# Optimization experiments

Measured on AMD Instinct MI355X. Metric: run time of the kernel, lower is better.

Reference implementation:

```python
import jax, jax.numpy as jnp
import numpy as np

N_TASK = 50000
N_EDGE = 50000
E = 500000
F_TASK = 64
F_EDGE = 64
H = 256
OUT = 256


def _lin(key, fan_in, fan_out):
    kw, kb = jax.random.split(key)
    lim = 1.0 / np.sqrt(fan_in)
    W = jax.random.uniform(kw, (fan_in, fan_out), minval=-lim, maxval=lim, dtype=jnp.float32)
    b = jax.random.uniform(kb, (fan_out,), minval=-lim, maxval=lim, dtype=jnp.float32)
    return W, b


def setup_inputs() -> dict:
    key = jax.random.key(0)
    ks = jax.random.split(key, 20)
    inp = {}
    inp['task_features'] = jax.random.normal(ks[0], (N_TASK, F_TASK), dtype=jnp.float32)
    inp['edge_features'] = jax.random.normal(ks[1], (N_EDGE, F_EDGE), dtype=jnp.float32)
    inp['queue_edges'] = jax.random.randint(ks[2], (2, E), 0, N_TASK)
    inp['type_edges'] = jax.random.randint(ks[3], (2, E), 0, N_TASK)
    inp['affinity_edges'] = jax.random.randint(ks[4], (2, E), 0, N_TASK)  # src<num_tasks, tgt<num_edges
    inp['topology_edges'] = jax.random.randint(ks[5], (2, E), 0, N_EDGE)
    inp['te_w1'], inp['te_b1'] = _lin(ks[6], F_TASK, H)
    inp['te_w2'], inp['te_b2'] = _lin(ks[7], H, H)
    inp['ee_w1'], inp['ee_b1'] = _lin(ks[8], F_EDGE, H)
    inp['ee_w2'], inp['ee_b2'] = _lin(ks[9], H, H)
    inp['gnn_w0'], inp['gnn_b0'] = _lin(ks[10], H, H)
    inp['gnn_w1'], inp['gnn_b1'] = _lin(ks[11], H, H)
    inp['ta_w'], inp['ta_b'] = _lin(ks[12], H, H)
    inp['ea_w'], inp['ea_b'] = _lin(ks[13], H, H)
    inp['out_w1'], inp['out_b1'] = _lin(ks[14], 2 * H, H)
    inp['out_w2'], inp['out_b2'] = _lin(ks[15], H, OUT)
    return inp


def _mean_msg(src_emb, src, tgt, num_segments):
    # scatter-add messages from src nodes into tgt slots, divide by in-degree (clamped >=1)
    msgs = jax.ops.segment_sum(src_emb[src], tgt, num_segments=num_segments)
    cnt = jax.ops.segment_sum(jnp.ones_like(src, dtype=src_emb.dtype), tgt, num_segments=num_segments)
    return msgs / jnp.maximum(cnt, 1.0)[:, None]


def _forward(task_features, edge_features, queue_edges, type_edges, affinity_edges, topology_edges,
             te_w1, te_b1, te_w2, te_b2, ee_w1, ee_b1, ee_w2, ee_b2,
             gnn_w0, gnn_b0, gnn_w1, gnn_b1, ta_w, ta_b, ea_w, ea_b,
             out_w1, out_b1, out_w2, out_b2):
    relu = jax.nn.relu
    # node encoders (Linear-ReLU-Linear-ReLU)
    t = relu(relu(task_features @ te_w1 + te_b1) @ te_w2 + te_b2)   # [N_task, H]
    e = relu(relu(edge_features @ ee_w1 + ee_b1) @ ee_w2 + ee_b2)   # [N_edge, H]

    # queue convolution: messages computed ONCE from original t (torch code never updates task_embeddings in loop)
    qs, qt = queue_edges[0], queue_edges[1]
    q_msgs = jax.ops.segment_sum(t[qs], qt, num_segments=t.shape[0])
    h = t
    for W, b in ((gnn_w0, gnn_b0), (gnn_w1, gnn_b1)):
        h = relu((h + 0.5 * q_msgs) @ W + b)
    t = h

    # type convolution: mean-aggregated same-type messages
    t = t + 0.3 * _mean_msg(t, type_edges[0], type_edges[1], t.shape[0])

    # affinity convolution: bipartite task<->edge exchange (simultaneous update)
    asrc, atgt = affinity_edges[0], affinity_edges[1]
    t_msgs = jax.ops.segment_sum(e[atgt], asrc, num_segments=t.shape[0])
    t_cnt = jax.ops.segment_sum(jnp.ones((asrc.shape[0],), t.dtype), asrc, num_segments=t.shape[0])
    e_msgs = jax.ops.segment_sum(t[asrc], atgt, num_segments=e.shape[0])
    e_cnt = jax.ops.segment_sum(jnp.ones((atgt.shape[0],), e.dtype), atgt, num_segments=e.shape[0])
    t_new = t + 0.3 * t_msgs / jnp.maximum(t_cnt, 1.0)[:, None]
    e_new = e + 0.3 * e_msgs / jnp.maximum(e_cnt, 1.0)[:, None]
    t, e = t_new, e_new

    # topology convolution: edge-edge mean aggregation
    e = e + 0.3 * _mean_msg(e, topology_edges[0], topology_edges[1], e.shape[0])

    # graph-level aggregation
    t_agg = relu(jnp.mean(t, axis=0) @ ta_w + ta_b)  # [H]
    e_agg = relu(jnp.mean(e, axis=0) @ ea_w + ea_b)  # [H]
    combined = jnp.concatenate([t_agg, e_agg], axis=0)  # [2H]
    out = relu(combined @ out_w1 + out_b1) @ out_w2 + out_b2  # [OUT]
    return out


def reference(task_features, edge_features, queue_edges, type_edges, affinity_edges, topology_edges,
              te_w1, te_b1, te_w2, te_b2, ee_w1, ee_b1, ee_w2, ee_b2,
              gnn_w0, gnn_b0, gnn_w1, gnn_b1, ta_w, ta_b, ea_w, ea_b,
              out_w1, out_b1, out_w2, out_b2):
    return _forward(task_features, edge_features, queue_edges, type_edges, affinity_edges, topology_edges,
                    te_w1, te_b1, te_w2, te_b2, ee_w1, ee_b1, ee_w2, ee_b2,
                    gnn_w0, gnn_b0, gnn_w1, gnn_b1, ta_w, ta_b, ea_w, ea_b,
                    out_w1, out_b1, out_w2, out_b2)
```

## Files before the change

### kernel.cpp

```cpp
#include <hip/hip_runtime.h>

#define H 256
#define NT 50000
#define NEDGE 50000
#define NE 500000

#define NBKT 391
#define NBLK 123
#define CHUNK 4096
#define CAP 2816

typedef __attribute__((ext_vector_type(8))) short short8_t;
typedef __attribute__((ext_vector_type(4))) float f32x4;
typedef unsigned short u16;
typedef unsigned int u32;

__device__ __forceinline__ float b2f(u16 v) { return __uint_as_float((u32)v << 16); }
__device__ __forceinline__ u16 f2b(float f) {
    u32 u = __float_as_uint(f);
    u += 0x7FFFu + ((u >> 16) & 1u);
    return (u16)(u >> 16);
}

__device__ __forceinline__ u32 f2fp8_1(float f) {
    u32 u = __float_as_uint(f);
    u32 s = (u >> 24) & 0x80u;
    float af = fabsf(f);
    if (af >= 448.f) return s | 0x7Eu;
    if (af < 0.015625f) {
        int m = (int)rintf(af * 512.0f);
        return s | (u32)m;
    }
    u32 au = __float_as_uint(af);
    u32 r = au + 0x7FFFFu + ((au >> 20) & 1u);
    int e = (int)(r >> 23) - 127;
    return s | (u32)(((e + 7) << 3) | ((r >> 20) & 7u));
}
__device__ __forceinline__ float fp82f_1(u32 b) {
    u32 s = (b & 0x80u) << 24;
    u32 em = b & 0x7Fu;
    float v;
    if (em >= 8) v = __uint_as_float((((em >> 3) + 120u) << 23) | ((em & 7u) << 20));
    else v = (float)em * 0.001953125f;
    return __uint_as_float(__float_as_uint(v) | s);
}
__device__ __forceinline__ u32 pk4_fp8(float a, float b, float c, float d) {
#if __has_builtin(__builtin_amdgcn_cvt_pk_fp8_f32)
    u32 r = 0;
    r = (u32)__builtin_amdgcn_cvt_pk_fp8_f32(a, b, (int)r, false);
    r = (u32)__builtin_amdgcn_cvt_pk_fp8_f32(c, d, (int)r, true);
    return r;
#else
    return f2fp8_1(a) | (f2fp8_1(b) << 8) | (f2fp8_1(c) << 16) | (f2fp8_1(d) << 24);
#endif
}
__device__ __forceinline__ float4 unpk4_fp8(u32 v) {
#if __has_builtin(__builtin_amdgcn_cvt_pk_f32_fp8)
    auto lo = __builtin_amdgcn_cvt_pk_f32_fp8(v, false);
    auto hi = __builtin_amdgcn_cvt_pk_f32_fp8(v, true);
    return make_float4(lo[0], lo[1], hi[0], hi[1]);
#else
    return make_float4(fp82f_1(v & 255u), fp82f_1((v >> 8) & 255u),
                       fp82f_1((v >> 16) & 255u), fp82f_1(v >> 24));
#endif
}

__device__ __forceinline__ const int* pick_list(
    int l, const int* a, const int* b, const int* c, const int* d, const int* e)
{ return (l == 0) ? a : (l == 1) ? b : (l == 2) ? c : (l == 3) ? d : e; }

__device__ __forceinline__ void enc_body(
    char* arena, int bid, const float* __restrict__ X,
    const u16* __restrict__ W1h, const u16* __restrict__ W1l, const float* __restrict__ b1,
    const u16* __restrict__ W2h, const u16* __restrict__ W2l, const float* __restrict__ b2,
    u16* __restrict__ out, u32* __restrict__ f8, int N)
{
    const int m0 = bid * 64;

    for (int i = threadIdx.x; i < 64 * 8; i += 256) {
        int r = i >> 3, c8 = i & 7;
        int gr = m0 + r; if (gr >= N) gr = N - 1;
        const float* xf = X + (size_t)gr * 64 + c8 * 8;
        float4 a = *(const float4*)xf;
        float4 b = *(const float4*)(xf + 4);
        uint4 v;
        v.x = (u32)f2b(a.x) | ((u32)f2b(a.y) << 16);
        v.y = (u32)f2b(a.z) | ((u32)f2b(a.w) << 16);
        v.z = (u32)f2b(b.x) | ((u32)f2b(b.y) << 16);
        v.w = (u32)f2b(b.z) | ((u32)f2b(b.w) << 16);
        u32 byte = (u32)(r * 128 + c8 * 16) ^ (u32)((r & 7) << 4);
        *(uint4*)(arena + byte) = v;
    }
    __syncthreads();

    const int wv = threadIdx.x >> 6, l = threadIdx.x & 63;
    const int li = l & 15, lk = l >> 4;

    f32x4 acc[4][4];
    #pragma unroll
    for (int i = 0; i < 4; i++)
        #pragma unroll
        for (int j = 0; j < 4; j++)
            acc[i][j] = (f32x4){0.f, 0.f, 0.f, 0.f};

    {
        short8_t whc[4], wlc[4];
        #pragma unroll
        for (int ni = 0; ni < 4; ni++) {
            const size_t wi = (size_t)((wv * 4 + ni) * 2) * 64 + l;
            whc[ni] = ((const short8_t*)W1h)[wi];
            wlc[ni] = ((const short8_t*)W1l)[wi];
        }
        #pragma unroll
        for (int ks = 0; ks < 2; ks++) {
            short8_t whn[4], wln[4];
            if (ks + 1 < 2) {
                #pragma unroll
                for (int ni = 0; ni < 4; ni++) {
                    const size_t wi = (size_t)((wv * 4 + ni) * 2 + ks + 1) * 64 + l;
                    whn[ni] = ((const short8_t*)W1h)[wi];
                    wln[ni] = ((const short8_t*)W1l)[wi];
                }
            }
            short8_t xb[4];
            #pragma unroll
            for (int mi = 0; mi < 4; mi++) {
                int m = mi * 16 + li;
                u32 byte = (u32)(m * 128 + (ks * 32 + lk * 8) * 2) ^ (u32)((m & 7) << 4);
                xb[mi] = *(const short8_t*)(arena + byte);
            }
            __builtin_amdgcn_s_setprio(1);
            #pragma unroll
            for (int ni = 0; ni < 4; ni++)
                #pragma unroll
                for (int mi = 0; mi < 4; mi++) {
                    acc[mi][ni] = __builtin_amdgcn_mfma_f32_16x16x32_bf16(wlc[ni], xb[mi], acc[mi][ni], 0, 0, 0);
                    acc[mi][ni] = __builtin_amdgcn_mfma_f32_16x16x32_bf16(whc[ni], xb[mi], acc[mi][ni], 0, 0, 0);
                }
            __builtin_amdgcn_s_setprio(0);
            if (ks + 1 < 2) {
                #pragma unroll
                for (int ni = 0; ni < 4; ni++) { whc[ni] = whn[ni]; wlc[ni] = wln[ni]; }
            }
        }
    }

    __syncthreads();

    #pragma unroll
    for (int ni = 0; ni < 4; ni++) {
        int c = wv * 64 + ni * 16 + lk * 4;
        float4 b4 = *(const float4*)(b1 + c);
        #pragma unroll
        for (int mi = 0; mi < 4; mi++) {
            int m = mi * 16 + li;
            float o0 = fmaxf(acc[mi][ni][0] + b4.x, 0.f);
            float o1 = fmaxf(acc[mi][ni][1] + b4.y, 0.f);
            float o2 = fmaxf(acc[mi][ni][2] + b4.z, 0.f);
            float o3 = fmaxf(acc[mi][ni][3] + b4.w, 0.f);
            u32 w0 = (u32)f2b(o0) | ((u32)f2b(o1) << 16);
            u32 w1 = (u32)f2b(o2) | ((u32)f2b(o3) << 16);
            u32 byte = (u32)(m * 512 + c * 2) ^ (u32)((m & 7) << 4);
            *(uint2*)(arena + byte) = make_uint2(w0, w1);
        }
    }
    __syncthreads();

    #pragma unroll
    for (int i = 0; i < 4; i++)
        #pragma unroll
        for (int j = 0; j < 4; j++)
            acc[i][j] = (f32x4){0.f, 0.f, 0.f, 0.f};

    {
        short8_t whc[4], wlc[4];
        #pragma unroll
        for (int ni = 0; ni < 4; ni++) {
            const size_t wi = (size_t)((wv * 4 + ni) * 8) * 64 + l;
            whc[ni] = ((const short8_t*)W2h)[wi];
            wlc[ni] = ((const short8_t*)W2l)[wi];
        }
        #pragma unroll
        for (int ks = 0; ks < 8; ks++) {
            short8_t whn[4], wln[4];
            if (ks + 1 < 8) {
                #pragma unroll
                for (int ni = 0; ni < 4; ni++) {
                    const size_t wi = (size_t)((wv * 4 + ni) * 8 + ks + 1) * 64 + l;
                    whn[ni] = ((const short8_t*)W2h)[wi];
                    wln[ni] = ((const short8_t*)W2l)[wi];
                }
            }
            short8_t xb[4];
            #pragma unroll
            for (int mi = 0; mi < 4; mi++) {
                int m = mi * 16 + li;
                u32 byte = (u32)(m * 512 + (ks * 32 + lk * 8) * 2) ^ (u32)((m & 7) << 4);
                xb[mi] = *(const short8_t*)(arena + byte);
            }
            __builtin_amdgcn_s_setprio(1);
            #pragma unroll
            for (int ni = 0; ni < 4; ni++)
                #pragma unroll
                for (int mi = 0; mi < 4; mi++) {
                    acc[mi][ni] = __builtin_amdgcn_mfma_f32_16x16x32_bf16(wlc[ni], xb[mi], acc[mi][ni], 0, 0, 0);
                    acc[mi][ni] = __builtin_amdgcn_mfma_f32_16x16x32_bf16(whc[ni], xb[mi], acc[mi][ni], 0, 0, 0);
                }
            __builtin_amdgcn_s_setprio(0);
            if (ks + 1 < 8) {
                #pragma unroll
                for (int ni = 0; ni < 4; ni++) { whc[ni] = whn[ni]; wlc[ni] = wln[ni]; }
            }
        }
    }

    __syncthreads();
    #pragma unroll
    for (int ni = 0; ni < 4; ni++) {
        int c = wv * 64 + ni * 16 + lk * 4;
        float4 b4 = *(const float4*)(b2 + c);
        #pragma unroll
        for (int mi = 0; mi < 4; mi++) {
            int m = mi * 16 + li;
            float o0 = fmaxf(acc[mi][ni][0] + b4.x, 0.f);
            float o1 = fmaxf(acc[mi][ni][1] + b4.y, 0.f);
            float o2 = fmaxf(acc[mi][ni][2] + b4.z, 0.f);
            float o3 = fmaxf(acc[mi][ni][3] + b4.w, 0.f);
            u32 w0 = (u32)f2b(o0) | ((u32)f2b(o1) << 16);
            u32 w1 = (u32)f2b(o2) | ((u32)f2b(o3) << 16);
            u32 byte = (u32)(m * 512 + c * 2) ^ (u32)((m & 7) << 4);
            *(uint2*)(arena + byte) = make_uint2(w0, w1);
        }
    }
    __syncthreads();
    for (int i = threadIdx.x; i < 64 * 32; i += 256) {
        int r = i >> 5, c8 = i & 31;
        int m = m0 + r;
        if (m < N) {
            u32 byte = (u32)(r * 512 + c8 * 16) ^ (u32)((r & 7) << 4);
            uint4 v = *(const uint4*)(arena + byte);
            *(uint4*)(out + (size_t)m * H + c8 * 8) = v;
            u32 p0 = pk4_fp8(b2f((u16)(v.x & 0xFFFF)), b2f((u16)(v.x >> 16)),
                             b2f((u16)(v.y & 0xFFFF)), b2f((u16)(v.y >> 16)));
            u32 p1 = pk4_fp8(b2f((u16)(v.z & 0xFFFF)), b2f((u16)(v.z >> 16)),
                             b2f((u16)(v.w & 0xFFFF)), b2f((u16)(v.w >> 16)));
            *(uint2*)(f8 + (size_t)m * 64 + c8 * 2) = make_uint2(p0, p1);
        }
    }
}

__global__ __launch_bounds__(256) void part_enc(
    const int* __restrict__ k0, const int* __restrict__ k1, const int* __restrict__ k2,
    const int* __restrict__ k3, const int* __restrict__ k4,
    const int* __restrict__ v0, const int* __restrict__ v1, const int* __restrict__ v2,
    const int* __restrict__ v3, const int* __restrict__ v4,
    const int* __restrict__ starts, int* __restrict__ csr,
    const float* __restrict__ X,
    const u16* __restrict__ W1h, const u16* __restrict__ W1l, const float* __restrict__ b1,
    const u16* __restrict__ W2h, const u16* __restrict__ W2l, const float* __restrict__ b2,
    u16* __restrict__ out, u32* __restrict__ f8, int N, int nCSR)
{
    __shared__ char arena[32768];
    if ((int)blockIdx.x >= nCSR) {
        enc_body(arena, blockIdx.x - nCSR, X, W1h, W1l, b1, W2h, W2l, b2, out, f8, N);
        return;
    }
    u32* ent = (u32*)arena;
    u16* ebk = (u16*)(arena + 16384);
    int* cnt  = (int*)(arena + 24576);
    int* loff = cnt + NBKT;
    int* cur  = loff + NBKT;
    int* gst  = cur + NBKT;
    int* buf  = (int*)(arena + 24576 + 4 * 4 * NBKT);
    int p = blockIdx.x;
    int l = p / NBLK, blk = p % NBLK;
    int t = threadIdx.x;
    const int* k = pick_list(l, k0, k1, k2, k3, k4);
    const int* v = pick_list(l, v0, v1, v2, v3, v4);
    const int* st = starts + ((size_t)l * NBLK + blk) * NBKT;
    for (int i = t; i < NBKT; i += 256) { cnt[i] = 0; gst[i] = st[i]; }
    __syncthreads();
    int e0 = blk * CHUNK;
    u32 ep[16]; int eb[16];
    #pragma unroll
    for (int j = 0; j < 16; j++) {
        int e = e0 + j * 256 + t;
        if (e < NE) {
            int key = k[e];
            eb[j] = key >> 7;
            ep[j] = ((u32)(key & 127) << 16) | (u32)v[e];
            atomicAdd(&cnt[eb[j]], 1);
        } else eb[j] = -1;
    }
    __syncthreads();
    int b0 = t * 2;
    int c0 = (b0 < NBKT) ? cnt[b0] : 0;
    int c1 = (b0 + 1 < NBKT) ? cnt[b0 + 1] : 0;
    int s = c0 + c1;
    buf[t] = s; __syncthreads();
    for (int stp = 1; stp < 256; stp <<= 1) {
        int x = (t >= stp) ? buf[t - stp] : 0; __syncthreads();
        buf[t] += x; __syncthreads();
    }
    int run = buf[t] - s;
    if (b0 < NBKT)     { loff[b0] = run;          cur[b0] = run; }
    if (b0 + 1 < NBKT) { loff[b0 + 1] = run + c0; cur[b0 + 1] = run + c0; }
    __syncthreads();
    #pragma unroll
    for (int j = 0; j < 16; j++) {
        if (eb[j] >= 0) {
            int q = atomicAdd(&cur[eb[j]], 1);
            ent[q] = ep[j]; ebk[q] = (u16)eb[j];
        }
    }
    __syncthreads();
    int nv = min(CHUNK, NE - e0);
    int* c = csr + (size_t)l * NE;
    for (int i = t; i < nv; i += 256) {
        int b = ebk[i];
        c[gst[b] + (i - loff[b])] = (int)ent[i];
    }
}

__global__ __launch_bounds__(256) void buck_enc(
    const int* __restrict__ bases, int* __restrict__ csr, int* __restrict__ off,
    const float* __restrict__ X,
    const u16* __restrict__ W1h, const u16* __restrict__ W1l, const float* __restrict__ b1,
    const u16* __restrict__ W2h, const u16* __restrict__ W2l, const float* __restrict__ b2,
    u16* __restrict__ out, u32* __restrict__ f8, int N, int nCSR)
{
    __shared__ char arena[32768];
    if ((int)blockIdx.x >= nCSR) {
        enc_body(arena, blockIdx.x - nCSR, X, W1h, W1l, b1, W2h, W2l, b2, out, f8, N);
        return;
    }
    int* seg  = (int*)arena;
    int* hist = (int*)(arena + 11264);
    int* scn  = hist + 128;
    int p = blockIdx.x;
    int l = p / NBKT, b = p % NBKT;
    int t = threadIdx.x;
    int base = bases[l * (NBKT + 1) + b];
    int end  = bases[l * (NBKT + 1) + b + 1];
    int sz = end - base; if (sz > CAP) sz = CAP;
    int* c = csr + (size_t)l * NE;
    for (int i = t; i < sz; i += 256) seg[i] = c[base + i];
    if (t < 128) hist[t] = 0;
    __syncthreads();
    for (int i = t; i < sz; i += 256) atomicAdd(&hist[seg[i] >> 16], 1);
    __syncthreads();
    if (t < 128) scn[t] = hist[t];
    __syncthreads();
    for (int st = 1; st < 128; st <<= 1) {
        int v = 0;
        if (t < 128 && t >= st) v = scn[t - st];
        __syncthreads();
        if (t < 128) scn[t] += v;
        __syncthreads();
    }
    if (t < 128) {
        int key = b * 128 + t;
        int excl = scn[t] - hist[t];
        if (key < NT) off[l * (NT + 1) + key] = base + excl;
        hist[t] = excl;
    }
    if (b == 0 && t == 128) off[l * (NT + 1) + NT] = NE;
    __syncthreads();
    for (int i = t; i < sz; i += 256) {
        int u = seg[i];
        int q = atomicAdd(&hist[u >> 16], 1);
        c[base + q] = u & 0xFFFF;
    }
}

template<int K1>
__global__ __launch_bounds__(256) void fused_mlp(
    const u16* __restrict__ X, const u16* __restrict__ Q,
    const u16* __restrict__ W1h, const u16* __restrict__ W1l, const float* __restrict__ b1,
    const u16* __restrict__ W2h, const u16* __restrict__ W2l, const float* __restrict__ b2,
    u16* __restrict__ out, u32* __restrict__ f8,
    int N, float s2)
{
    __shared__ u16 lds[64 * 256];
    const int m0 = blockIdx.x * 64;

    constexpr int RCH = K1 / 8;
    for (int i = threadIdx.x; i < 64 * RCH; i += 256) {
        int r = i / RCH, c8 = i % RCH;
        int gr = m0 + r; if (gr >= N) gr = N - 1;
        uint4 v = *(const uint4*)(X + (size_t)gr * K1 + c8 * 8);
        u32 byte = (u32)(r * (K1 * 2) + c8 * 16) ^ (u32)((r & 7) << 4);
        *(uint4*)((char*)lds + byte) = v;
    }
    __syncthreads();

    const int wv = threadIdx.x >> 6, l = threadIdx.x & 63;
    const int li = l & 15, lk = l >> 4;

    f32x4 acc[4][4];
    #pragma unroll
    for (int i = 0; i < 4; i++)
        #pragma unroll
        for (int j = 0; j < 4; j++)
            acc[i][j] = (f32x4){0.f, 0.f, 0.f, 0.f};

    {
        constexpr int KS = K1 / 32;
        short8_t whc[4], wlc[4];
        #pragma unroll
        for (int ni = 0; ni < 4; ni++) {
            const size_t wi = (size_t)((wv * 4 + ni) * KS) * 64 + l;
            whc[ni] = ((const short8_t*)W1h)[wi];
            wlc[ni] = ((const short8_t*)W1l)[wi];
        }
        #pragma unroll
        for (int ks = 0; ks < KS; ks++) {
            short8_t whn[4], wln[4];
            if (ks + 1 < KS) {
                #pragma unroll
                for (int ni = 0; ni < 4; ni++) {
                    const size_t wi = (size_t)((wv * 4 + ni) * KS + ks + 1) * 64 + l;
                    whn[ni] = ((const short8_t*)W1h)[wi];
                    wln[ni] = ((const short8_t*)W1l)[wi];
                }
            }
            short8_t xb[4];
            #pragma unroll
            for (int mi = 0; mi < 4; mi++) {
                int m = mi * 16 + li;
                u32 byte = (u32)(m * (K1 * 2) + (ks * 32 + lk * 8) * 2) ^ (u32)((m & 7) << 4);
                xb[mi] = *(const short8_t*)((const char*)lds + byte);
            }
            __builtin_amdgcn_s_setprio(1);
            #pragma unroll
            for (int ni = 0; ni < 4; ni++)
                #pragma unroll
                for (int mi = 0; mi < 4; mi++) {
                    acc[mi][ni] = __builtin_amdgcn_mfma_f32_16x16x32_bf16(wlc[ni], xb[mi], acc[mi][ni], 0, 0, 0);
                    acc[mi][ni] = __builtin_amdgcn_mfma_f32_16x16x32_bf16(whc[ni], xb[mi], acc[mi][ni], 0, 0, 0);
                }
            __builtin_amdgcn_s_setprio(0);
            if (ks + 1 < KS) {
                #pragma unroll
                for (int ni = 0; ni < 4; ni++) { whc[ni] = whn[ni]; wlc[ni] = wln[ni]; }
            }
        }
    }

    __syncthreads();

    #pragma unroll
    for (int ni = 0; ni < 4; ni++) {
        int c = wv * 64 + ni * 16 + lk * 4;
        float4 b4 = *(const float4*)(b1 + c);
        #pragma unroll
        for (int mi = 0; mi < 4; mi++) {
            int m = mi * 16 + li;
            float o0 = fmaxf(acc[mi][ni][0] + b4.x, 0.f);
            float o1 = fmaxf(acc[mi][ni][1] + b4.y, 0.f);
            float o2 = fmaxf(acc[mi][ni][2] + b4.z, 0.f);
            float o3 = fmaxf(acc[mi][ni][3] + b4.w, 0.f);
            int gm = m0 + m; if (gm >= N) gm = N - 1;
            uint2 qv = *(const uint2*)(Q + (size_t)gm * 256 + c);
            o0 = fmaf(s2, b2f((u16)(qv.x & 0xFFFF)), o0);
            o1 = fmaf(s2, b2f((u16)(qv.x >> 16)), o1);
            o2 = fmaf(s2, b2f((u16)(qv.y & 0xFFFF)), o2);
            o3 = fmaf(s2, b2f((u16)(qv.y >> 16)), o3);
            u32 w0 = (u32)f2b(o0) | ((u32)f2b(o1) << 16);
            u32 w1 = (u32)f2b(o2) | ((u32)f2b(o3) << 16);
            u32 byte = (u32)(m * 512 + c * 2) ^ (u32)((m & 7) << 4);
            *(uint2*)((char*)lds + byte) = make_uint2(w0, w1);
        }
    }
    __syncthreads();

    #pragma unroll
    for (int i = 0; i < 4; i++)
        #pragma unroll
        for (int j = 0; j < 4; j++)
            acc[i][j] = (f32x4){0.f, 0.f, 0.f, 0.f};

    {
        short8_t whc[4], wlc[4];
        #pragma unroll
        for (int ni = 0; ni < 4; ni++) {
            const size_t wi = (size_t)((wv * 4 + ni) * 8) * 64 + l;
            whc[ni] = ((const short8_t*)W2h)[wi];
            wlc[ni] = ((const short8_t*)W2l)[wi];
        }
        #pragma unroll
        for (int ks = 0; ks < 8; ks++) {
            short8_t whn[4], wln[4];
            if (ks + 1 < 8) {
                #pragma unroll
                for (int ni = 0; ni < 4; ni++) {
                    const size_t wi = (size_t)((wv * 4 + ni) * 8 + ks + 1) * 64 + l;
                    whn[ni] = ((const short8_t*)W2h)[wi];
                    wln[ni] = ((const short8_t*)W2l)[wi];
                }
            }
            short8_t xb[4];
            #pragma unroll
            for (int mi = 0; mi < 4; mi++) {
                int m = mi * 16 + li;
                u32 byte = (u32)(m * 512 + (ks * 32 + lk * 8) * 2) ^ (u32)((m & 7) << 4);
                xb[mi] = *(const short8_t*)((const char*)lds + byte);
            }
            __builtin_amdgcn_s_setprio(1);
            #pragma unroll
            for (int ni = 0; ni < 4; ni++)
                #pragma unroll
                for (int mi = 0; mi < 4; mi++) {
                    acc[mi][ni] = __builtin_amdgcn_mfma_f32_16x16x32_bf16(wlc[ni], xb[mi], acc[mi][ni], 0, 0, 0);
                    acc[mi][ni] = __builtin_amdgcn_mfma_f32_16x16x32_bf16(whc[ni], xb[mi], acc[mi][ni], 0, 0, 0);
                }
            __builtin_amdgcn_s_setprio(0);
            if (ks + 1 < 8) {
                #pragma unroll
                for (int ni = 0; ni < 4; ni++) { whc[ni] = whn[ni]; wlc[ni] = wln[ni]; }
            }
        }
    }

    __syncthreads();
    #pragma unroll
    for (int ni = 0; ni < 4; ni++) {
        int c = wv * 64 + ni * 16 + lk * 4;
        float4 b4 = *(const float4*)(b2 + c);
        #pragma unroll
        for (int mi = 0; mi < 4; mi++) {
            int m = mi * 16 + li;
            float o0 = fmaxf(acc[mi][ni][0] + b4.x, 0.f);
            float o1 = fmaxf(acc[mi][ni][1] + b4.y, 0.f);
            float o2 = fmaxf(acc[mi][ni][2] + b4.z, 0.f);
            float o3 = fmaxf(acc[mi][ni][3] + b4.w, 0.f);
            u32 w0 = (u32)f2b(o0) | ((u32)f2b(o1) << 16);
            u32 w1 = (u32)f2b(o2) | ((u32)f2b(o3) << 16);
            u32 byte = (u32)(m * 512 + c * 2) ^ (u32)((m & 7) << 4);
            *(uint2*)((char*)lds + byte) = make_uint2(w0, w1);
        }
    }
    __syncthreads();
    for (int i = threadIdx.x; i < 64 * 32; i += 256) {
        int r = i >> 5, c8 = i & 31;
        int m = m0 + r;
        if (m < N) {
            u32 byte = (u32)(r * 512 + c8 * 16) ^ (u32)((r & 7) << 4);
            uint4 v = *(const uint4*)((const char*)lds + byte);
            *(uint4*)(out + (size_t)m * H + c8 * 8) = v;
            u32 p0 = pk4_fp8(b2f((u16)(v.x & 0xFFFF)), b2f((u16)(v.x >> 16)),
                             b2f((u16)(v.y & 0xFFFF)), b2f((u16)(v.y >> 16)));
            u32 p1 = pk4_fp8(b2f((u16)(v.z & 0xFFFF)), b2f((u16)(v.z >> 16)),
                             b2f((u16)(v.w & 0xFFFF)), b2f((u16)(v.w >> 16)));
            *(uint2*)(f8 + (size_t)m * 64 + c8 * 2) = make_uint2(p0, p1);
        }
    }
}

__global__ __launch_bounds__(256) void wt_pack(
    const float* __restrict__ s0, const float* __restrict__ s1,
    const float* __restrict__ s2, const float* __restrict__ s3,
    const float* __restrict__ s4, const float* __restrict__ s5,
    u16* __restrict__ arena)
{
    const int li = blockIdx.y;
    const int K = (li == 0 || li == 4) ? 64 : 256;
    const int offs[6] = {0, 32768, 163840, 294912, 425984, 458752};
    int n = K * 256;
    int i = blockIdx.x * 256 + threadIdx.x;
    if (i >= n) return;
    const float* W = (li == 0) ? s0 : (li == 1) ? s1 : (li == 2) ? s2
                   : (li == 3) ? s3 : (li == 4) ? s4 : s5;
    u16* hi = arena + offs[li];
    u16* lo = hi + n;
    int k = i >> 8, c = i & 255;
    float u = W[i];
    u32 b = __float_as_uint(u);
    float r = u - __uint_as_float(b & 0xFFFF0000u);
    int lane = ((k >> 3) & 3) * 16 + (c & 15);
    size_t idx = ((size_t)((c >> 4) * (K >> 5) + (k >> 5)) * 64 + lane) * 8 + (k & 7);
    hi[idx] = (u16)(b >> 16);
    lo[idx] = f2b(r);
}

__global__ __launch_bounds__(256) void hist_kernel(
    const int* __restrict__ k0, const int* __restrict__ k1, const int* __restrict__ k2,
    const int* __restrict__ k3, const int* __restrict__ k4, int* __restrict__ counts)
{
    __shared__ int h[NBKT];
    int l = blockIdx.y;
    const int* k = pick_list(l, k0, k1, k2, k3, k4);
    for (int i = threadIdx.x; i < NBKT; i += 256) h[i] = 0;
    __syncthreads();
    int e0 = blockIdx.x * CHUNK;
    for (int i = threadIdx.x; i < CHUNK; i += 256) {
        int e = e0 + i;
        if (e < NE) atomicAdd(&h[k[e] >> 7], 1);
    }
    __syncthreads();
    int* out = counts + ((size_t)l * NBLK + blockIdx.x) * NBKT;
    for (int i = threadIdx.x; i < NBKT; i += 256) out[i] = h[i];
}

__global__ __launch_bounds__(256) void scan_buckets(
    const int* __restrict__ counts, int* __restrict__ starts, int* __restrict__ bases)
{
    __shared__ int buf[256];
    int l = blockIdx.x, t = threadIdx.x;
    const int* cl = counts + (size_t)l * NBLK * NBKT;
    int* sl = starts + (size_t)l * NBLK * NBKT;
    int b0 = t * 2;
    int totloc[2];
    int s = 0;
    #pragma unroll
    for (int j = 0; j < 2; j++) {
        int b = b0 + j, v = 0;
        if (b < NBKT) for (int k = 0; k < NBLK; k++) v += cl[k * NBKT + b];
        totloc[j] = v; s += v;
    }
    buf[t] = s; __syncthreads();
    for (int st = 1; st < 256; st <<= 1) {
        int v = (t >= st) ? buf[t - st] : 0; __syncthreads();
        buf[t] += v; __syncthreads();
    }
    int run = buf[t] - s;
    #pragma unroll
    for (int j = 0; j < 2; j++) {
        int b = b0 + j;
        if (b < NBKT) {
            bases[l * (NBKT + 1) + b] = run;
            int p = run;
            for (int k = 0; k < NBLK; k++) { sl[k * NBKT + b] = p; p += cl[k * NBKT + b]; }
            run += totloc[j];
        }
    }
    if (t == 255) bases[l * (NBKT + 1) + NBKT] = NE;
}

__global__ __launch_bounds__(256) void gather_q_f8(
    const u32* __restrict__ src, const int* __restrict__ csr,
    const int* __restrict__ off, const u16* __restrict__ baseT,
    u16* __restrict__ sumOut, u16* __restrict__ fuseOut, float s2, int N)
{
    int r = (blockIdx.x * 256 + threadIdx.x) >> 6;
    int lane = threadIdx.x & 63;
    if (r >= N) return;
    int o0 = off[r];
    int d  = off[r + 1] - o0;
    float4 acc = {0.f, 0.f, 0.f, 0.f};
    int j = 0;
    for (; j + 8 <= d; j += 8) {
        u32 w[8];
        #pragma unroll
        for (int q = 0; q < 8; q++)
            w[q] = src[(size_t)csr[o0 + j + q] * 64 + lane];
        #pragma unroll
        for (int q = 0; q < 8; q++) {
            float4 f = unpk4_fp8(w[q]);
            acc.x += f.x; acc.y += f.y; acc.z += f.z; acc.w += f.w;
        }
    }
    for (; j < d; j++) {
        float4 f = unpk4_fp8(src[(size_t)csr[o0 + j] * 64 + lane]);
        acc.x += f.x; acc.y += f.y; acc.z += f.z; acc.w += f.w;
    }
    ushort4 pk;
    pk.x = f2b(acc.x); pk.y = f2b(acc.y); pk.z = f2b(acc.z); pk.w = f2b(acc.w);
    ((ushort4*)(sumOut + (size_t)r * H))[lane] = pk;
    ushort4 b = ((const ushort4*)(baseT + (size_t)r * H))[lane];
    pk.x = f2b(fmaf(s2, acc.x, b2f(b.x)));
    pk.y = f2b(fmaf(s2, acc.y, b2f(b.y)));
    pk.z = f2b(fmaf(s2, acc.z, b2f(b.z)));
    pk.w = f2b(fmaf(s2, acc.w, b2f(b.w)));
    ((ushort4*)(fuseOut + (size_t)r * H))[lane] = pk;
}

__global__ __launch_bounds__(256) void gather_task2(
    const u32* __restrict__ M1s, const int* __restrict__ csr1, const int* __restrict__ off1,
    const u32* __restrict__ M2s, const int* __restrict__ csr2, const int* __restrict__ off2,
    const u16* __restrict__ T, u16* __restrict__ Sout, u32* __restrict__ M3out, int N)
{
    int r = (blockIdx.x * 256 + threadIdx.x) >> 6;
    int lane = threadIdx.x & 63;
    if (r >= N) return;

    float4 a1 = {0.f, 0.f, 0.f, 0.f};
    {
        int o0 = off1[r], d = off1[r + 1] - o0;
        int j = 0;
        for (; j + 8 <= d; j += 8) {
            u32 w[8];
            #pragma unroll
            for (int q = 0; q < 8; q++)
                w[q] = M1s[(size_t)csr1[o0 + j + q] * 64 + lane];
            #pragma unroll
            for (int q = 0; q < 8; q++) {
                float4 f = unpk4_fp8(w[q]);
                a1.x += f.x; a1.y += f.y; a1.z += f.z; a1.w += f.w;
            }
        }
        for (; j < d; j++) {
            float4 f = unpk4_fp8(M1s[(size_t)csr1[o0 + j] * 64 + lane]);
            a1.x += f.x; a1.y += f.y; a1.z += f.z; a1.w += f.w;
        }
        float s = 0.3f / (float)max(d, 1);
        a1.x *= s; a1.y *= s; a1.z *= s; a1.w *= s;
    }
    float4 a2 = {0.f, 0.f, 0.f, 0.f};
    {
        int o0 = off2[r], d = off2[r + 1] - o0;
        int j = 0;
        for (; j + 8 <= d; j += 8) {
            u32 w[8];
            #pragma unroll
            for (int q = 0; q < 8; q++)
                w[q] = M2s[(size_t)csr2[o0 + j + q] * 64 + lane];
            #pragma unroll
            for (int q = 0; q < 8; q++) {
                float4 f = unpk4_fp8(w[q]);
                a2.x += f.x; a2.y += f.y; a2.z += f.z; a2.w += f.w;
            }
        }
        for (; j < d; j++) {
            float4 f = unpk4_fp8(M2s[(size_t)csr2[o0 + j] * 64 + lane]);
            a2.x += f.x; a2.y += f.y; a2.z += f.z; a2.w += f.w;
        }
        float s = 0.3f / (float)max(d, 1);
        a2.x *= s; a2.y *= s; a2.z *= s; a2.w *= s;
    }
    ushort4 b = ((const ushort4*)(T + (size_t)r * H))[lane];
    float f0 = b2f(b.x) + a1.x, f1 = b2f(b.y) + a1.y;
    float f2 = b2f(b.z) + a1.z, f3 = b2f(b.w) + a1.w;
    M3out[(size_t)r * 64 + lane] = pk4_fp8(f0, f1, f2, f3);
    ushort4 pk;
    pk.x = f2b(f0 + a2.x); pk.y = f2b(f1 + a2.y);
    pk.z = f2b(f2 + a2.z); pk.w = f2b(f3 + a2.w);
    ((ushort4*)(Sout + (size_t)r * H))[lane] = pk;
}

__global__ __launch_bounds__(256) void gather_mean_f8(
    const u32* __restrict__ src, const int* __restrict__ csr, const int* __restrict__ off,
    const u16* __restrict__ base, u16* __restrict__ dst, u32* __restrict__ m8,
    float alpha, int N)
{
    int r = (blockIdx.x * 256 + threadIdx.x) >> 6;
    int lane = threadIdx.x & 63;
    if (r >= N) return;
    int o0 = off[r];
    int d  = off[r + 1] - o0;
    float4 acc = {0.f, 0.f, 0.f, 0.f};
    int j = 0;
    for (; j + 8 <= d; j += 8) {
        u32 w[8];
        #pragma unroll
        for (int q = 0; q < 8; q++)
            w[q] = src[(size_t)csr[o0 + j + q] * 64 + lane];
        #pragma unroll
        for (int q = 0; q < 8; q++) {
            float4 f = unpk4_fp8(w[q]);
            acc.x += f.x; acc.y += f.y; acc.z += f.z; acc.w += f.w;
        }
    }
    for (; j < d; j++) {
        float4 f = unpk4_fp8(src[(size_t)csr[o0 + j] * 64 + lane]);
        acc.x += f.x; acc.y += f.y; acc.z += f.z; acc.w += f.w;
    }
    float s = alpha / (float)max(d, 1);
    ushort4 b = ((const ushort4*)(base + (size_t)r * H))[lane];
    float o0f = fmaf(s, acc.x, b2f(b.x));
    float o1f = fmaf(s, acc.y, b2f(b.y));
    float o2f = fmaf(s, acc.z, b2f(b.z));
    float o3f = fmaf(s, acc.w, b2f(b.w));
    ushort4 pk;
    pk.x = f2b(o0f); pk.y = f2b(o1f); pk.z = f2b(o2f); pk.w = f2b(o3f);
    ((ushort4*)(dst + (size_t)r * H))[lane] = pk;
    if (m8) m8[(size_t)r * 64 + lane] = pk4_fp8(o0f, o1f, o2f, o3f);
}

__global__ __launch_bounds__(256) void colsum_slots(
    const u16* __restrict__ embA, const u16* __restrict__ embB,
    float* __restrict__ part, int N)
{
    int blk = blockIdx.x;
    const u16* emb = (blk < 256) ? embA : embB;
    int rb = blk & 255;
    int c = threadIdx.x;
    float s = 0.f;
    for (int r = rb; r < N; r += 256)
        s += b2f(emb[(size_t)r * H + c]);
    part[(size_t)blk * H + c] = s;
}

__global__ __launch_bounds__(256) void head_comb(
    const float* __restrict__ part, float invNT, float invNE,
    const float* __restrict__ ta_w, const float* __restrict__ ta_b,
    const float* __restrict__ ea_w, const float* __restrict__ ea_b,
    float* __restrict__ comb)
{
    __shared__ float mean[H];
    __shared__ float red[32][8];
    int blk = blockIdx.x;
    int side = blk >> 3;
    int c0 = (blk & 7) * 32;
    int t = threadIdx.x;
    const float* p = part + (side ? (size_t)256 * H : 0);
    float s = 0.f;
    for (int b = 0; b < 256; b++) s += p[(size_t)b * H + t];
    mean[t] = s * (side ? invNE : invNT);
    __syncthreads();
    const float* W = side ? ea_w : ta_w;
    const float* bb = side ? ea_b : ta_b;
    int c = t & 31, g = t >> 5;
    float acc = 0.f;
    for (int k = g * 32; k < g * 32 + 32; k++)
        acc += mean[k] * W[k * H + (c0 + c)];
    red[c][g] = acc;
    __syncthreads();
    if (t < 32) {
        float v = 0.f;
        #pragma unroll
        for (int g2 = 0; g2 < 8; g2++) v += red[t][g2];
        comb[side * H + c0 + t] = fmaxf(v + bb[c0 + t], 0.f);
    }
}

__global__ __launch_bounds__(256) void head_hid(
    const float* __restrict__ comb, const float* __restrict__ ow1,
    const float* __restrict__ ob1, float* __restrict__ hid)
{
    __shared__ float cb[2 * H];
    __shared__ float red[32][8];
    int c0 = blockIdx.x * 32;
    int t = threadIdx.x;
    cb[t] = comb[t];
    cb[t + H] = comb[t + H];
    __syncthreads();
    int c = t & 31, g = t >> 5;
    float acc = 0.f;
    for (int k = g * 64; k < g * 64 + 64; k++)
        acc += cb[k] * ow1[k * H + (c0 + c)];
    red[c][g] = acc;
    __syncthreads();
    if (t < 32) {
        float v = 0.f;
        #pragma unroll
        for (int g2 = 0; g2 < 8; g2++) v += red[t][g2];
        hid[c0 + t] = fmaxf(v + ob1[c0 + t], 0.f);
    }
}

__global__ __launch_bounds__(256) void head_out(
    const float* __restrict__ hid, const float* __restrict__ ow2,
    const float* __restrict__ ob2, float* __restrict__ out)
{
    __shared__ float hb[H];
    __shared__ float red[32][8];
    int c0 = blockIdx.x * 32;
    int t = threadIdx.x;
    hb[t] = hid[t];
    __syncthreads();
    int c = t & 31, g = t >> 5;
    float acc = 0.f;
    for (int k = g * 32; k < g * 32 + 32; k++)
        acc += hb[k] * ow2[k * H + (c0 + c)];
    red[c][g] = acc;
    __syncthreads();
    if (t < 32) {
        float v = 0.f;
        #pragma unroll
        for (int g2 = 0; g2 < 8; g2++) v += red[t][g2];
        out[c0 + t] = v + ob2[c0 + t];
    }
}

extern "C" void kernel_launch(void* const* d_in, const int* in_sizes, int n_in,
                              void* d_out, int out_size, void* d_ws, size_t ws_size,
                              hipStream_t stream) {
    const float* tf  = (const float*)d_in[0];
    const float* ef  = (const float*)d_in[1];
    const int*   qe  = (const int*)d_in[2];
    const int*   te  = (const int*)d_in[3];
    const int*   ae  = (const int*)d_in[4];
    const int*   pe  = (const int*)d_in[5];
    const float* te_w1 = (const float*)d_in[6];  const float* te_b1 = (const float*)d_in[7];
    const float* te_w2 = (const float*)d_in[8];  const float* te_b2 = (const float*)d_in[9];
    const float* ee_w1 = (const float*)d_in[10]; const float* ee_b1 = (const float*)d_in[11];
    const float* ee_w2 = (const float*)d_in[12]; const float* ee_b2 = (const float*)d_in[13];
    const float* gw0 = (const float*)d_in[14];   const float* gb0 = (const float*)d_in[15];
    const float* gw1 = (const float*)d_in[16];   const float* gb1 = (const float*)d_in[17];
    const float* ta_w = (const float*)d_in[18];  const float* ta_b = (const float*)d_in[19];
    const float* ea_w = (const float*)d_in[20];  const float* ea_b = (const float*)d_in[21];
    const float* ow1 = (const float*)d_in[22];   const float* ob1 = (const float*)d_in[23];
    const float* ow2 = (const float*)d_in[24];   const float* ob2 = (const float*)d_in[25];

    const size_t NB = (size_t)NT * H;
    u16* T  = (u16*)d_ws;
    u16* Bf = T + NB;
    u16* S  = Bf + NB;
    u16* F  = S + NB;
    float* sumpad = (float*)(F + NB);
    int* off5   = (int*)(sumpad + 2 * H);
    int* csr5   = off5 + 5 * (NT + 1);
    int* counts = csr5 + (size_t)5 * NE;
    int* starts = counts + (size_t)5 * NBLK * NBKT;
    int* bases  = starts + (size_t)5 * NBLK * NBKT;
    u32* M0 = (u32*)(((size_t)(bases + 5 * (NBKT + 1)) + 15) & ~(size_t)15);
    u32* M1 = M0 + NB / 4;
    u32* M2 = M1 + NB / 4;
    u32* M3 = M2 + NB / 4;
    u32* M4 = M3 + NB / 4;
    float* part = (float*)(M4 + NB / 4);
    u16* warena = (u16*)(((size_t)(part + 512 * 256) + 15) & ~(size_t)15);
    u16* wt_te1_h = warena + 0;      u16* wt_te1_l = warena + 16384;
    u16* wt_te2_h = warena + 32768;  u16* wt_te2_l = warena + 98304;
    u16* wt_g0_h  = warena + 163840; u16* wt_g0_l  = warena + 229376;
    u16* wt_g1_h  = warena + 294912; u16* wt_g1_l  = warena + 360448;
    u16* wt_ee1_h = warena + 425984; u16* wt_ee1_l = warena + 442368;
    u16* wt_ee2_h = warena + 458752; u16* wt_ee2_l = warena + 524288;
    float* comb = (float*)(warena + 589824);
    float* hidb = comb + 2 * H;

    const int MG = (NT + 63) / 64;
    const int GB = (NT * 64) / 256;
    const int NPART = NBLK * 5;
    const int NBUCK = NBKT * 5;

    const int *k0 = qe + NE, *k1 = te + NE, *k2 = ae,      *k3 = ae + NE, *k4 = pe + NE;
    const int *v0 = qe,      *v1 = te,      *v2 = ae + NE, *v3 = ae,      *v4 = pe;

    wt_pack<<<dim3(256, 6), 256, 0, stream>>>(te_w1, te_w2, gw0, gw1, ee_w1, ee_w2, warena);
    hist_kernel<<<dim3(NBLK, 5), 256, 0, stream>>>(k0, k1, k2, k3, k4, counts);
    scan_buckets<<<5, 256, 0, stream>>>(counts, starts, bases);

    part_enc<<<NPART + MG, 256, 0, stream>>>(
        k0, k1, k2, k3, k4, v0, v1, v2, v3, v4, starts, csr5,
        tf, wt_te1_h, wt_te1_l, te_b1, wt_te2_h, wt_te2_l, te_b2, T, M0, NT, NPART);

    buck_enc<<<NBUCK + MG, 256, 0, stream>>>(
        bases, csr5, off5,
        ef, wt_ee1_h, wt_ee1_l, ee_b1, wt_ee2_h, wt_ee2_l, ee_b2, Bf, M2, NT, NBUCK);

    #define LOFF(l) (off5 + (l) * (NT + 1))
    #define LCSR(l) (csr5 + (size_t)(l) * NE)

    gather_q_f8<<<GB, 256, 0, stream>>>(M0, LCSR(0), LOFF(0), T, S, F, 0.5f, NT);

    fused_mlp<256><<<MG, 256, 0, stream>>>(
        F, S, wt_g0_h, wt_g0_l, gb0, wt_g1_h, wt_g1_l, gb1, T, M1, NT, 0.5f);

    gather_task2<<<GB, 256, 0, stream>>>(
        M1, LCSR(1), LOFF(1), M2, LCSR(2), LOFF(2), T, S, M3, NT);

    gather_mean_f8<<<GB, 256, 0, stream>>>(
        M3, LCSR(3), LOFF(3), Bf, F, M4, 0.3f, NT);

    gather_mean_f8<<<GB, 256, 0, stream>>>(
        M4, LCSR(4), LOFF(4), F, Bf, nullptr, 0.3f, NT);

    colsum_slots<<<512, 256, 0, stream>>>(S, Bf, part, NT);
    head_comb<<<16, 256, 0, stream>>>(part, 1.f / NT, 1.f / NEDGE,
                                      ta_w, ta_b, ea_w, ea_b, comb);
    head_hid<<<8, 256, 0, stream>>>(comb, ow1, ob1, hidb);
    head_out<<<8, 256, 0, stream>>>(hidb, ow2, ob2, (float*)d_out);
}
```

Measured before the change: 405.4 us.

## Store queue-message sum as fp8 and merge gather_task2 neighbor loops

The queue aggregation sum passed from gather_q_f8 to fused_mlp is now stored as packed fp8 instead of bf16, halving the bytes written and re-read for that intermediate. gather_task2 walks both adjacency lists in one loop with combined batches of 8, so more loads are in flight for low-degree rows and there is less tail handling. Mean scaling is folded into fmas. Storing the sum in fp8 adds quantization error to the residual term fed into the MLP.

```diff
diff --git a/kernel.cpp b/kernel.cpp
--- a/kernel.cpp
+++ b/kernel.cpp
@@ -375,7 +375,7 @@
 
 template<int K1>
 __global__ __launch_bounds__(256) void fused_mlp(
-    const u16* __restrict__ X, const u16* __restrict__ Q,
+    const u16* __restrict__ X, const u32* __restrict__ Q8,
     const u16* __restrict__ W1h, const u16* __restrict__ W1l, const float* __restrict__ b1,
     const u16* __restrict__ W2h, const u16* __restrict__ W2l, const float* __restrict__ b2,
     u16* __restrict__ out, u32* __restrict__ f8,
@@ -461,11 +461,11 @@
             float o2 = fmaxf(acc[mi][ni][2] + b4.z, 0.f);
             float o3 = fmaxf(acc[mi][ni][3] + b4.w, 0.f);
             int gm = m0 + m; if (gm >= N) gm = N - 1;
-            uint2 qv = *(const uint2*)(Q + (size_t)gm * 256 + c);
-            o0 = fmaf(s2, b2f((u16)(qv.x & 0xFFFF)), o0);
-            o1 = fmaf(s2, b2f((u16)(qv.x >> 16)), o1);
-            o2 = fmaf(s2, b2f((u16)(qv.y & 0xFFFF)), o2);
-            o3 = fmaf(s2, b2f((u16)(qv.y >> 16)), o3);
+            float4 qf = unpk4_fp8(Q8[(size_t)gm * 64 + (c >> 2)]);
+            o0 = fmaf(s2, qf.x, o0);
+            o1 = fmaf(s2, qf.y, o1);
+            o2 = fmaf(s2, qf.z, o2);
+            o3 = fmaf(s2, qf.w, o3);
             u32 w0 = (u32)f2b(o0) | ((u32)f2b(o1) << 16);
             u32 w1 = (u32)f2b(o2) | ((u32)f2b(o3) << 16);
             u32 byte = (u32)(m * 512 + c * 2) ^ (u32)((m & 7) << 4);
@@ -640,7 +640,7 @@
 __global__ __launch_bounds__(256) void gather_q_f8(
     const u32* __restrict__ src, const int* __restrict__ csr,
     const int* __restrict__ off, const u16* __restrict__ baseT,
-    u16* __restrict__ sumOut, u16* __restrict__ fuseOut, float s2, int N)
+    u32* __restrict__ S8out, u16* __restrict__ fuseOut, float s2, int N)
 {
     int r = (blockIdx.x * 256 + threadIdx.x) >> 6;
     int lane = threadIdx.x & 63;
@@ -664,10 +664,9 @@
         float4 f = unpk4_fp8(src[(size_t)csr[o0 + j] * 64 + lane]);
         acc.x += f.x; acc.y += f.y; acc.z += f.z; acc.w += f.w;
     }
+    S8out[(size_t)r * 64 + lane] = pk4_fp8(acc.x, acc.y, acc.z, acc.w);
+    ushort4 b = ((const ushort4*)(baseT + (size_t)r * H))[lane];
     ushort4 pk;
-    pk.x = f2b(acc.x); pk.y = f2b(acc.y); pk.z = f2b(acc.z); pk.w = f2b(acc.w);
-    ((ushort4*)(sumOut + (size_t)r * H))[lane] = pk;
-    ushort4 b = ((const ushort4*)(baseT + (size_t)r * H))[lane];
     pk.x = f2b(fmaf(s2, acc.x, b2f(b.x)));
     pk.y = f2b(fmaf(s2, acc.y, b2f(b.y)));
     pk.z = f2b(fmaf(s2, acc.z, b2f(b.z)));
@@ -684,57 +683,38 @@
     int lane = threadIdx.x & 63;
     if (r >= N) return;
 
+    int o1 = off1[r], d1 = off1[r + 1] - o1;
+    int o2 = off2[r], d2 = off2[r + 1] - o2;
+    int tot = d1 + d2;
     float4 a1 = {0.f, 0.f, 0.f, 0.f};
-    {
-        int o0 = off1[r], d = off1[r + 1] - o0;
-        int j = 0;
-        for (; j + 8 <= d; j += 8) {
-            u32 w[8];
-            #pragma unroll
-            for (int q = 0; q < 8; q++)
-                w[q] = M1s[(size_t)csr1[o0 + j + q] * 64 + lane];
-            #pragma unroll
-            for (int q = 0; q < 8; q++) {
-                float4 f = unpk4_fp8(w[q]);
-                a1.x += f.x; a1.y += f.y; a1.z += f.z; a1.w += f.w;
-            }
-        }
-        for (; j < d; j++) {
-            float4 f = unpk4_fp8(M1s[(size_t)csr1[o0 + j] * 64 + lane]);
-            a1.x += f.x; a1.y += f.y; a1.z += f.z; a1.w += f.w;
-        }
-        float s = 0.3f / (float)max(d, 1);
-        a1.x *= s; a1.y *= s; a1.z *= s; a1.w *= s;
-    }
     float4 a2 = {0.f, 0.f, 0.f, 0.f};
-    {
-        int o0 = off2[r], d = off2[r + 1] - o0;
-        int j = 0;
-        for (; j + 8 <= d; j += 8) {
-            u32 w[8];
-            #pragma unroll
-            for (int q = 0; q < 8; q++)
-                w[q] = M2s[(size_t)csr2[o0 + j + q] * 64 + lane];
-            #pragma unroll
-            for (int q = 0; q < 8; q++) {
-                float4 f = unpk4_fp8(w[q]);
-                a2.x += f.x; a2.y += f.y; a2.z += f.z; a2.w += f.w;
-            }
-        }
-        for (; j < d; j++) {
-            float4 f = unpk4_fp8(M2s[(size_t)csr2[o0 + j] * 64 + lane]);
-            a2.x += f.x; a2.y += f.y; a2.z += f.z; a2.w += f.w;
-        }
-        float s = 0.3f / (float)max(d, 1);
-        a2.x *= s; a2.y *= s; a2.z *= s; a2.w *= s;
-    }
+
+    for (int base = 0; base < tot; base += 8) {
+        u32 w[8];
+        #pragma unroll
+        for (int q = 0; q < 8; q++) {
+            int idx = base + q;
+            if (idx < d1)       w[q] = M1s[(size_t)csr1[o1 + idx] * 64 + lane];
+            else if (idx < tot) w[q] = M2s[(size_t)csr2[o2 + idx - d1] * 64 + lane];
+        }
+        #pragma unroll
+        for (int q = 0; q < 8; q++) {
+            int idx = base + q;
+            if (idx >= tot) break;
+            float4 f = unpk4_fp8(w[q]);
+            if (idx < d1) { a1.x += f.x; a1.y += f.y; a1.z += f.z; a1.w += f.w; }
+            else          { a2.x += f.x; a2.y += f.y; a2.z += f.z; a2.w += f.w; }
+        }
+    }
+    float s1 = 0.3f / (float)max(d1, 1);
+    float s2 = 0.3f / (float)max(d2, 1);
     ushort4 b = ((const ushort4*)(T + (size_t)r * H))[lane];
-    float f0 = b2f(b.x) + a1.x, f1 = b2f(b.y) + a1.y;
-    float f2 = b2f(b.z) + a1.z, f3 = b2f(b.w) + a1.w;
+    float f0 = fmaf(s1, a1.x, b2f(b.x)), f1 = fmaf(s1, a1.y, b2f(b.y));
+    float f2 = fmaf(s1, a1.z, b2f(b.z)), f3 = fmaf(s1, a1.w, b2f(b.w));
     M3out[(size_t)r * 64 + lane] = pk4_fp8(f0, f1, f2, f3);
     ushort4 pk;
-    pk.x = f2b(f0 + a2.x); pk.y = f2b(f1 + a2.y);
-    pk.z = f2b(f2 + a2.z); pk.w = f2b(f3 + a2.w);
+    pk.x = f2b(fmaf(s2, a2.x, f0)); pk.y = f2b(fmaf(s2, a2.y, f1));
+    pk.z = f2b(fmaf(s2, a2.z, f2)); pk.w = f2b(fmaf(s2, a2.w, f3));
     ((ushort4*)(Sout + (size_t)r * H))[lane] = pk;
 }
 
@@ -898,6 +878,7 @@
     u16* Bf = T + NB;
     u16* S  = Bf + NB;
     u16* F  = S + NB;
+    u32* S8 = (u32*)S;
     float* sumpad = (float*)(F + NB);
     int* off5   = (int*)(sumpad + 2 * H);
     int* csr5   = off5 + 5 * (NT + 1);
@@ -943,10 +924,10 @@
     #define LOFF(l) (off5 + (l) * (NT + 1))
     #define LCSR(l) (csr5 + (size_t)(l) * NE)
 
-    gather_q_f8<<<GB, 256, 0, stream>>>(M0, LCSR(0), LOFF(0), T, S, F, 0.5f, NT);
+    gather_q_f8<<<GB, 256, 0, stream>>>(M0, LCSR(0), LOFF(0), T, S8, F, 0.5f, NT);
 
     fused_mlp<256><<<MG, 256, 0, stream>>>(
-        F, S, wt_g0_h, wt_g0_l, gb0, wt_g1_h, wt_g1_l, gb1, T, M1, NT, 0.5f);
+        F, S8, wt_g0_h, wt_g0_l, gb0, wt_g1_h, wt_g1_l, gb1, T, M1, NT, 0.5f);
 
     gather_task2<<<GB, 256, 0, stream>>>(
         M1, LCSR(1), LOFF(1), M2, LCSR(2), LOFF(2), T, S, M3, NT);
```

Result: slower. 428.8 us (+5.8%).
